# Performance work log

Measured on AMD Instinct MI355X. Metric: run time of the kernel, lower is better.

The kernel has to match this reference:

```python
import jax, jax.numpy as jnp
import numpy as np

# mamba-130m config (n_layers reduced to 4 for the reference baseline)
V, Dm, NL, Di, Ns, K, R = 50280, 768, 4, 1536, 16, 4, 48

def rmsnorm(x, w, eps=1e-5):
    return x * jax.lax.rsqrt(jnp.mean(x * x, axis=-1, keepdims=True) + eps) * w

def mixer(r, in_w, conv_w, conv_b, x_w, dt_w, dt_b, A_log, Dp, out_w):
    Bsz, L, _ = r.shape
    xz = jnp.einsum('bld,ed->ble', r, in_w)            # [B,L,2*Di]
    x, z = jnp.split(xz, 2, axis=-1)
    # depthwise causal conv1d, kernel K
    xp = jnp.pad(x, ((0, 0), (K - 1, 0), (0, 0)))
    x = sum(conv_w[:, k] * xp[:, k:k + L] for k in range(K)) + conv_b
    x = jax.nn.silu(x)
    proj = jnp.einsum('bld,ed->ble', x, x_w)           # [B,L,R+2*Ns]
    dt_r, Bm, Cm = proj[..., :R], proj[..., R:R + Ns], proj[..., R + Ns:]
    dt = jax.nn.softplus(jnp.einsum('blr,dr->bld', dt_r, dt_w) + dt_b)  # [B,L,Di]
    A = -jnp.exp(A_log)                                # [Di,Ns]
    dA = jnp.exp(dt[..., None] * A)                    # [B,L,Di,Ns]
    dBx = dt[..., None] * Bm[:, :, None, :] * x[..., None]
    def step(h, xs):
        dA_t, dBx_t, C_t = xs
        h = dA_t * h + dBx_t                           # [B,Di,Ns]
        return h, jnp.einsum('bdn,bn->bd', h, C_t)
    h0 = jnp.zeros((Bsz, Di, Ns), r.dtype)
    _, ys = jax.lax.scan(step, h0, (dA.transpose(1, 0, 2, 3), dBx.transpose(1, 0, 2, 3), Cm.transpose(1, 0, 2)))
    y = ys.transpose(1, 0, 2) + Dp * x
    y = y * jax.nn.silu(z)
    return jnp.einsum('ble,de->bld', y, out_w)

def mamba_logits(ids, mask, embed, in_proj_w, conv_w, conv_b, x_proj_w, dt_proj_w, dt_proj_b, A_log, Dp, out_proj_w, norm_w, final_norm_w):
    h = embed[ids] * mask[..., None].astype(embed.dtype)
    for l in range(NL):
        h = h + mixer(rmsnorm(h, norm_w[l]), in_proj_w[l], conv_w[l], conv_b[l],
                      x_proj_w[l], dt_proj_w[l], dt_proj_b[l], A_log[l], Dp[l], out_proj_w[l])
    h = rmsnorm(h, final_norm_w)
    return jnp.einsum('bld,vd->blv', h, embed)  # tied lm_head

def setup_inputs() -> dict:
    key = jax.random.key(0)
    ks = jax.random.split(key, 12)
    s = 0.02
    B, Lq, La = 2, 512, 128
    dt_b0 = float(np.log(np.expm1(0.01)))  # softplus^{-1}(0.01)
    return {
        'question_ids': jax.random.randint(ks[0], (B, Lq), 0, V, dtype=jnp.int64),
        'question_mask': jnp.ones((B, Lq), dtype=jnp.int32),
        'answer_ids': jax.random.randint(ks[1], (B, La), 0, V, dtype=jnp.int64),
        'answer_mask': jnp.ones((B, La), dtype=jnp.int32),
        'embed': jax.random.normal(ks[2], (V, Dm), jnp.float32) * s,
        'in_proj_w': jax.random.normal(ks[3], (NL, 2 * Di, Dm), jnp.float32) * s,
        'conv_w': jax.random.normal(ks[4], (NL, Di, K), jnp.float32) * s,
        'conv_b': jnp.zeros((NL, Di), jnp.float32),
        'x_proj_w': jax.random.normal(ks[5], (NL, R + 2 * Ns, Di), jnp.float32) * s,
        'dt_proj_w': jax.random.normal(ks[6], (NL, Di, R), jnp.float32) * s,
        'dt_proj_b': jnp.full((NL, Di), dt_b0, jnp.float32),
        'A_log': jnp.broadcast_to(jnp.log(jnp.arange(1, Ns + 1, dtype=jnp.float32)), (NL, Di, Ns)).copy(),
        'Dp': jnp.ones((NL, Di), jnp.float32),
        'out_proj_w': jax.random.normal(ks[7], (NL, Dm, Di), jnp.float32) * s,
        'norm_w': jnp.ones((NL, Dm), jnp.float32),
        'final_norm_w': jnp.ones((Dm,), jnp.float32),
    }

def reference(question_ids, question_mask, answer_ids, answer_mask, embed, in_proj_w, conv_w, conv_b, x_proj_w, dt_proj_w, dt_proj_b, A_log, Dp, out_proj_w, norm_w, final_norm_w):
    # answer_ids/answer_mask are unused by the original forward as well.
    return mamba_logits(question_ids, question_mask, embed, in_proj_w, conv_w, conv_b,
                        x_proj_w, dt_proj_w, dt_proj_b, A_log, Dp, out_proj_w, norm_w, final_norm_w)
```

## Files before the change

### kernel.cpp

```cpp
#include <hip/hip_runtime.h>

#define DI 1536
#define DM 768
#define NS 16
#define RK 48
#define LQ 512
#define BB 2
#define MROWS (BB*LQ)

typedef unsigned short u16;
typedef short bf16x8 __attribute__((ext_vector_type(8)));
typedef float f32x4 __attribute__((ext_vector_type(4)));
typedef u16 u16x8 __attribute__((ext_vector_type(8)));

static __device__ __forceinline__ short f2bf(float f) {
  unsigned u = __float_as_uint(f);
  u += 0x7FFF + ((u >> 16) & 1);
  return (short)(u >> 16);
}

static __device__ __forceinline__ void gld16(const void* g, void* l) {
  __builtin_amdgcn_global_load_lds((const __attribute__((address_space(1))) unsigned int*)g,
                                   (__attribute__((address_space(3))) unsigned int*)l,
                                   16, 0, 0);
}

__global__ __launch_bounds__(256) void k_cast8(const float* __restrict__ s,
                                               u16* __restrict__ d, long n) {
  long i = ((long)blockIdx.x * 256 + threadIdx.x) * 8;
  if (i >= n) return;
  float4 a = *(const float4*)(s + i);
  float4 b = *(const float4*)(s + i + 4);
  u16x8 o;
  o[0] = (u16)f2bf(a.x); o[1] = (u16)f2bf(a.y); o[2] = (u16)f2bf(a.z); o[3] = (u16)f2bf(a.w);
  o[4] = (u16)f2bf(b.x); o[5] = (u16)f2bf(b.y); o[6] = (u16)f2bf(b.z); o[7] = (u16)f2bf(b.w);
  *(u16x8*)(d + i) = o;
}

__global__ __launch_bounds__(256) void k_gather(const int* __restrict__ ids,
                                                const int* __restrict__ mask,
                                                const float* __restrict__ embed,
                                                float* __restrict__ h) {
  int row = blockIdx.x;
  int id = ids[row];
  float mk = (float)mask[row];
  const float* src = embed + (size_t)id * DM;
  float* dst = h + (size_t)row * DM;
  for (int i = threadIdx.x; i < DM; i += 256) dst[i] = src[i] * mk;
}

__global__ __launch_bounds__(256) void k_rmsnorm(const float* __restrict__ h,
                                                 const float* __restrict__ w,
                                                 u16* __restrict__ out) {
  int row = blockIdx.x;
  const float* x = h + (size_t)row * DM;
  int tid = threadIdx.x;
  float v0 = x[tid], v1 = x[tid + 256], v2 = x[tid + 512];
  float ss = v0*v0 + v1*v1 + v2*v2;
  #pragma unroll
  for (int o = 32; o > 0; o >>= 1) ss += __shfl_xor(ss, o);
  __shared__ float ps[4];
  if ((tid & 63) == 0) ps[tid >> 6] = ss;
  __syncthreads();
  float tot = ps[0] + ps[1] + ps[2] + ps[3];
  float scale = rsqrtf(tot * (1.0f/768.0f) + 1e-5f);
  u16* o0 = out + (size_t)row * DM;
  o0[tid]       = (u16)f2bf(v0 * scale * w[tid]);
  o0[tid + 256] = (u16)f2bf(v1 * scale * w[tid + 256]);
  o0[tid + 512] = (u16)f2bf(v2 * scale * w[tid + 512]);
}

template<int WM, int WN, int TM, int TN, bool RES>
__global__ __launch_bounds__(256) void k_gemm_bf(const u16* __restrict__ A,
                                                 const u16* __restrict__ B,
                                                 float* __restrict__ C,
                                                 int M, int N, int K) {
  constexpr int BM = WM*TM*16, BN = WN*TN*16, BK = 32;
  __shared__ __attribute__((aligned(16))) u16 As[BM*BK];
  __shared__ __attribute__((aligned(16))) u16 Bs[BN*BK];

  int bx, by;
  {
    int CT = gridDim.x, RT = gridDim.y;
    int lin = blockIdx.y * CT + blockIdx.x;
    int CT8 = CT & ~7;
    int main_n = CT8 * RT;
    if (lin < main_n) {
      int x = lin & 7, g = lin >> 3;
      by = g % RT;
      bx = x + 8 * (g / RT);
    } else {
      int rem = lin - main_n;
      by = rem % RT;
      bx = CT8 + rem / RT;
    }
  }

  const int m0 = by * BM, n0 = bx * BN;
  const int tid = threadIdx.x;
  const int wave = tid >> 6, lane = tid & 63;
  const int wm = (wave / WN) * (TM*16), wn = (wave % WN) * (TN*16);
  const int lm = lane & 15, q = lane >> 4;
  const int srow = tid >> 2;
  const int ssub = (tid & 3) * 8;

  f32x4 acc[TM][TN] = {};
  for (int kt = 0; kt < K; kt += BK) {
    __syncthreads();
    #pragma unroll
    for (int i = 0; i < BM/64; i++) {
      const u16* g = A + (size_t)(m0 + i*64 + srow)*K + kt + ssub;
      gld16(g, (void*)(As + (i*256 + wave*64)*8));
    }
    #pragma unroll
    for (int i = 0; i < BN/64; i++) {
      int bn = n0 + i*64 + srow;
      if (bn > N-1) bn = N-1;
      const u16* g = B + (size_t)bn*K + kt + ssub;
      gld16(g, (void*)(Bs + (i*256 + wave*64)*8));
    }
    __syncthreads();
    bf16x8 af[TM], bfr[TN];
    #pragma unroll
    for (int i = 0; i < TM; i++)
      af[i] = *(const bf16x8*)(&As[(wm + i*16 + lm)*BK + q*8]);
    #pragma unroll
    for (int j = 0; j < TN; j++)
      bfr[j] = *(const bf16x8*)(&Bs[(wn + j*16 + lm)*BK + q*8]);
    #pragma unroll
    for (int i = 0; i < TM; i++)
      #pragma unroll
      for (int j = 0; j < TN; j++)
        acc[i][j] = __builtin_amdgcn_mfma_f32_16x16x32_bf16(af[i], bfr[j], acc[i][j], 0, 0, 0);
  }
  #pragma unroll
  for (int i = 0; i < TM; i++) {
    #pragma unroll
    for (int j = 0; j < TN; j++) {
      int rm = m0 + wm + i*16 + q*4;
      int cn = n0 + wn + j*16 + lm;
      if (cn < N) {
        float* cp = C + (size_t)rm*N + cn;
        #pragma unroll
        for (int r2 = 0; r2 < 4; r2++) {
          float v = acc[i][j][r2];
          if (RES) v += cp[(size_t)r2*N];
          cp[(size_t)r2*N] = v;
        }
      }
    }
  }
}

__global__ __launch_bounds__(256) void k_conv(const float* __restrict__ xz,
                                              const float* __restrict__ cw,
                                              const float* __restrict__ cb,
                                              float* __restrict__ xs) {
  int idx = blockIdx.x * 256 + threadIdx.x;
  int d = idx % DI;
  int t = (idx / DI) % LQ;
  int b = idx / (DI * LQ);
  const float* xcol = xz + (size_t)b * LQ * (2*DI) + d;
  float acc = cb[d];
  #pragma unroll
  for (int k = 0; k < 4; k++) {
    int tt = t + k - 3;
    if (tt >= 0) acc += cw[d*4 + k] * xcol[(size_t)tt * (2*DI)];
  }
  float s = acc / (1.0f + expf(-acc));
  xs[idx] = s;
}

__global__ __launch_bounds__(256) void k_proj(const float* __restrict__ xs,
                                              const float* __restrict__ w,
                                              float* __restrict__ proj) {
  int wave = threadIdx.x >> 6, lane = threadIdx.x & 63;
  int m = blockIdx.x * 4 + wave;
  const float* xr = xs + (size_t)m * DI;
  float xv[24];
  #pragma unroll
  for (int j = 0; j < 24; j++) xv[j] = xr[lane + j*64];
  for (int n = 0; n < 80; n++) {
    const float* wr = w + (size_t)n * DI;
    float acc = 0.f;
    #pragma unroll
    for (int j = 0; j < 24; j++) acc += xv[j] * wr[lane + j*64];
    #pragma unroll
    for (int o = 32; o > 0; o >>= 1) acc += __shfl_xor(acc, o);
    if (lane == 0) proj[(size_t)m * 80 + n] = acc;
  }
}

__global__ __launch_bounds__(256) void k_dt(const float* __restrict__ proj,
                                            const float* __restrict__ dtw,
                                            const float* __restrict__ dtb,
                                            float* __restrict__ dt) {
  int m = blockIdx.y;
  int d = blockIdx.x * 256 + threadIdx.x;
  __shared__ float p[RK];
  if (threadIdx.x < RK) p[threadIdx.x] = proj[(size_t)m * 80 + threadIdx.x];
  __syncthreads();
  const float* wr = dtw + (size_t)d * RK;
  float acc = dtb[d];
  #pragma unroll
  for (int r = 0; r < RK; r++) acc += p[r] * wr[r];
  float sp = (acc > 20.f) ? acc : log1pf(expf(acc));
  dt[(size_t)m * DI + d] = sp;
}

#define SCT 32
__global__ __launch_bounds__(256) void k_scan(const float* __restrict__ dt,
                                              const float* __restrict__ proj,
                                              const float* __restrict__ xs,
                                              const float* __restrict__ A_log,
                                              float* __restrict__ y) {
  const int d = blockIdx.x;
  const int b = blockIdx.y;
  const int tid = threadIdx.x;
  const int n = tid & 15;
  const int c = tid >> 4;
  const int t0 = c * SCT;
  const float negA = -expf(A_log[d * NS + n]);
  const float* dtp = dt   + (size_t)b * LQ * DI + d;
  const float* xp  = xs   + (size_t)b * LQ * DI + d;
  const float* Bp  = proj + (size_t)b * LQ * 80 + RK + n;
  const float* Cp  = proj + (size_t)b * LQ * 80 + RK + NS + n;

  float a[SCT], u[SCT], Cv[SCT];
  #pragma unroll
  for (int j = 0; j < SCT; j++) {
    int t = t0 + j;
    float dtv = dtp[(size_t)t * DI];
    float xv  = xp[(size_t)t * DI];
    float Bv  = Bp[(size_t)t * 80];
    Cv[j]     = Cp[(size_t)t * 80];
    a[j] = expf(dtv * negA);
    u[j] = dtv * Bv * xv;
  }
  float P = 1.f, H = 0.f;
  #pragma unroll
  for (int j = 0; j < SCT; j++) { H = a[j]*H + u[j]; P *= a[j]; }

  __shared__ float Ps[16][16], Hs[16][16], Ss[16][16];
  Ps[c][n] = P; Hs[c][n] = H;
  __syncthreads();
  if (tid < 16) {
    float S = 0.f;
    #pragma unroll
    for (int cc = 0; cc < 16; cc++) {
      Ss[cc][tid] = S;
      S = Ps[cc][tid] * S + Hs[cc][tid];
    }
  }
  __syncthreads();

  float h = Ss[c][n];
  float* yp = y + (size_t)b * LQ * DI + d;
  #pragma unroll
  for (int j = 0; j < SCT; j++) {
    h = a[j]*h + u[j];
    float yy = h * Cv[j];
    yy += __shfl_xor(yy, 1);
    yy += __shfl_xor(yy, 2);
    yy += __shfl_xor(yy, 4);
    yy += __shfl_xor(yy, 8);
    if (n == 0) yp[(size_t)(t0 + j) * DI] = yy;
  }
}

__global__ __launch_bounds__(256) void k_gate(const float* __restrict__ y,
                                              const float* __restrict__ xs,
                                              const float* __restrict__ xz,
                                              const float* __restrict__ Dp,
                                              u16* __restrict__ yb) {
  int idx = blockIdx.x * 256 + threadIdx.x;
  int d = idx % DI;
  int bt = idx / DI;
  float zv = xz[(size_t)bt * (2*DI) + DI + d];
  float sz = zv / (1.0f + expf(-zv));
  float v = (y[idx] + Dp[d] * xs[idx]) * sz;
  yb[idx] = (u16)f2bf(v);
}

extern "C" void kernel_launch(void* const* d_in, const int* in_sizes, int n_in,
                              void* d_out, int out_size, void* d_ws, size_t ws_size,
                              hipStream_t stream) {
  const int*   q_ids        = (const int*)d_in[0];
  const int*   q_mask       = (const int*)d_in[1];
  const float* embed        = (const float*)d_in[4];
  const float* in_proj_w    = (const float*)d_in[5];
  const float* conv_w       = (const float*)d_in[6];
  const float* conv_b       = (const float*)d_in[7];
  const float* x_proj_w     = (const float*)d_in[8];
  const float* dt_proj_w    = (const float*)d_in[9];
  const float* dt_proj_b    = (const float*)d_in[10];
  const float* A_log        = (const float*)d_in[11];
  const float* Dp           = (const float*)d_in[12];
  const float* out_proj_w   = (const float*)d_in[13];
  const float* norm_w       = (const float*)d_in[14];
  const float* final_norm_w = (const float*)d_in[15];
  float* out = (float*)d_out;

  float* ws = (float*)d_ws;
  float* h   = ws;
  float* xz  = h  + 786432;
  float* xs  = xz + 3145728;
  float* pj  = xs + 1572864;
  float* dtb = pj + 81920;
  float* y   = dtb + 1572864;
  u16*   rb  = (u16*)(y + 1572864);
  u16*   yb  = rb  + 786432;
  u16*   ipw = yb  + 1572864;
  u16*   opw = ipw + 9437184;
  u16*   emb = opw + 4718592;

  k_cast8<<<4608, 256, 0, stream>>>(in_proj_w, ipw, 9437184L);
  k_cast8<<<2304, 256, 0, stream>>>(out_proj_w, opw, 4718592L);
  k_cast8<<<18855, 256, 0, stream>>>(embed, emb, 38615040L);

  k_gather<<<MROWS, 256, 0, stream>>>(q_ids, q_mask, embed, h);

  for (int l = 0; l < 4; l++) {
    k_rmsnorm<<<MROWS, 256, 0, stream>>>(h, norm_w + (size_t)l*DM, rb);
    k_gemm_bf<1,4,4,2,false><<<dim3(3072/128, MROWS/64), 256, 0, stream>>>(
        rb, ipw + (size_t)l*2359296, xz, MROWS, 2*DI, DM);
    k_conv<<<(MROWS*DI)/256, 256, 0, stream>>>(xz, conv_w + (size_t)l*DI*4,
                                               conv_b + (size_t)l*DI, xs);
    k_proj<<<MROWS/4, 256, 0, stream>>>(xs, x_proj_w + (size_t)l*80*DI, pj);
    k_dt<<<dim3(DI/256, MROWS), 256, 0, stream>>>(pj, dt_proj_w + (size_t)l*DI*RK,
                                                  dt_proj_b + (size_t)l*DI, dtb);
    k_scan<<<dim3(DI, BB), 256, 0, stream>>>(dtb, pj, xs,
                                             A_log + (size_t)l*DI*NS, y);
    k_gate<<<(MROWS*DI)/256, 256, 0, stream>>>(y, xs, xz, Dp + (size_t)l*DI, yb);
    k_gemm_bf<2,2,2,2,true><<<dim3(DM/64, MROWS/64), 256, 0, stream>>>(
        yb, opw + (size_t)l*1179648, h, MROWS, DM, DI);
  }

  k_rmsnorm<<<MROWS, 256, 0, stream>>>(h, final_norm_w, rb);
  k_gemm_bf<2,2,4,4,false><<<dim3((50280 + 127)/128, MROWS/128), 256, 0, stream>>>(
      rb, emb, out, MROWS, 50280, 768);
}
```

Before: 1.537 ms.

## Double-buffer GEMM LDS tiles and fuse dt projection and gating into scan

The GEMM kernel now uses two LDS buffers and issues the async global-to-LDS load for the next K tile before computing on the current one. This is meant to overlap memory latency with MFMA work and cut one barrier per iteration. Separately, the dt projection plus softplus is computed inside the scan block into shared memory, and the D-skip plus SiLU gate with the bf16 store is folded into the scan output loop. That removes two kernel launches and the dt/y intermediate buffers, but each scan block recomputes dt for all 512 timesteps. There is also a possible race: the next-tile async loads are issued without waiting on completion before the barrier.

```diff
diff --git a/kernel.cpp b/kernel.cpp
--- a/kernel.cpp
+++ b/kernel.cpp
@@ -76,8 +76,8 @@
                                                  float* __restrict__ C,
                                                  int M, int N, int K) {
   constexpr int BM = WM*TM*16, BN = WN*TN*16, BK = 32;
-  __shared__ __attribute__((aligned(16))) u16 As[BM*BK];
-  __shared__ __attribute__((aligned(16))) u16 Bs[BN*BK];
+  __shared__ __attribute__((aligned(16))) u16 As[2][BM*BK];
+  __shared__ __attribute__((aligned(16))) u16 Bs[2][BN*BK];
 
   int bx, by;
   {
@@ -104,34 +104,41 @@
   const int srow = tid >> 2;
   const int ssub = (tid & 3) * 8;
 
-  f32x4 acc[TM][TN] = {};
-  for (int kt = 0; kt < K; kt += BK) {
-    __syncthreads();
+  auto stage = [&](int buf, int kt) {
     #pragma unroll
     for (int i = 0; i < BM/64; i++) {
       const u16* g = A + (size_t)(m0 + i*64 + srow)*K + kt + ssub;
-      gld16(g, (void*)(As + (i*256 + wave*64)*8));
+      gld16(g, (void*)(As[buf] + (i*256 + wave*64)*8));
     }
     #pragma unroll
     for (int i = 0; i < BN/64; i++) {
       int bn = n0 + i*64 + srow;
       if (bn > N-1) bn = N-1;
       const u16* g = B + (size_t)bn*K + kt + ssub;
-      gld16(g, (void*)(Bs + (i*256 + wave*64)*8));
-    }
-    __syncthreads();
+      gld16(g, (void*)(Bs[buf] + (i*256 + wave*64)*8));
+    }
+  };
+
+  f32x4 acc[TM][TN] = {};
+  const int nt = K / BK;
+  stage(0, 0);
+  __syncthreads();
+  for (int t = 0; t < nt; ++t) {
+    const int cur = t & 1;
+    if (t + 1 < nt) stage(cur ^ 1, (t + 1) * BK);
     bf16x8 af[TM], bfr[TN];
     #pragma unroll
     for (int i = 0; i < TM; i++)
-      af[i] = *(const bf16x8*)(&As[(wm + i*16 + lm)*BK + q*8]);
+      af[i] = *(const bf16x8*)(&As[cur][(wm + i*16 + lm)*BK + q*8]);
     #pragma unroll
     for (int j = 0; j < TN; j++)
-      bfr[j] = *(const bf16x8*)(&Bs[(wn + j*16 + lm)*BK + q*8]);
+      bfr[j] = *(const bf16x8*)(&Bs[cur][(wn + j*16 + lm)*BK + q*8]);
     #pragma unroll
     for (int i = 0; i < TM; i++)
       #pragma unroll
       for (int j = 0; j < TN; j++)
         acc[i][j] = __builtin_amdgcn_mfma_f32_16x16x32_bf16(af[i], bfr[j], acc[i][j], 0, 0, 0);
+    __syncthreads();
   }
   #pragma unroll
   for (int i = 0; i < TM; i++) {
@@ -191,46 +198,47 @@
   }
 }
 
-__global__ __launch_bounds__(256) void k_dt(const float* __restrict__ proj,
-                                            const float* __restrict__ dtw,
-                                            const float* __restrict__ dtb,
-                                            float* __restrict__ dt) {
-  int m = blockIdx.y;
-  int d = blockIdx.x * 256 + threadIdx.x;
-  __shared__ float p[RK];
-  if (threadIdx.x < RK) p[threadIdx.x] = proj[(size_t)m * 80 + threadIdx.x];
-  __syncthreads();
-  const float* wr = dtw + (size_t)d * RK;
-  float acc = dtb[d];
-  #pragma unroll
-  for (int r = 0; r < RK; r++) acc += p[r] * wr[r];
-  float sp = (acc > 20.f) ? acc : log1pf(expf(acc));
-  dt[(size_t)m * DI + d] = sp;
-}
-
 #define SCT 32
-__global__ __launch_bounds__(256) void k_scan(const float* __restrict__ dt,
-                                              const float* __restrict__ proj,
+__global__ __launch_bounds__(256) void k_scan(const float* __restrict__ proj,
                                               const float* __restrict__ xs,
+                                              const float* __restrict__ xz,
                                               const float* __restrict__ A_log,
-                                              float* __restrict__ y) {
+                                              const float* __restrict__ dtw,
+                                              const float* __restrict__ dtbp,
+                                              const float* __restrict__ Dp,
+                                              u16* __restrict__ yb) {
   const int d = blockIdx.x;
   const int b = blockIdx.y;
   const int tid = threadIdx.x;
   const int n = tid & 15;
   const int c = tid >> 4;
   const int t0 = c * SCT;
+
+  __shared__ float dt_s[LQ];
+  const float* pjb = proj + (size_t)b * LQ * 80;
+  {
+    const float* wr = dtw + (size_t)d * RK;
+    float dtb0 = dtbp[d];
+    for (int t = tid; t < LQ; t += 256) {
+      const float* pr = pjb + (size_t)t * 80;
+      float acc = dtb0;
+      #pragma unroll
+      for (int r = 0; r < RK; r++) acc += pr[r] * wr[r];
+      dt_s[t] = (acc > 20.f) ? acc : log1pf(expf(acc));
+    }
+  }
+  __syncthreads();
+
   const float negA = -expf(A_log[d * NS + n]);
-  const float* dtp = dt   + (size_t)b * LQ * DI + d;
-  const float* xp  = xs   + (size_t)b * LQ * DI + d;
-  const float* Bp  = proj + (size_t)b * LQ * 80 + RK + n;
-  const float* Cp  = proj + (size_t)b * LQ * 80 + RK + NS + n;
+  const float* xp  = xs + (size_t)b * LQ * DI + d;
+  const float* Bp  = pjb + RK + n;
+  const float* Cp  = pjb + RK + NS + n;
 
   float a[SCT], u[SCT], Cv[SCT];
   #pragma unroll
   for (int j = 0; j < SCT; j++) {
     int t = t0 + j;
-    float dtv = dtp[(size_t)t * DI];
+    float dtv = dt_s[t];
     float xv  = xp[(size_t)t * DI];
     float Bv  = Bp[(size_t)t * 80];
     Cv[j]     = Cp[(size_t)t * 80];
@@ -255,7 +263,9 @@
   __syncthreads();
 
   float h = Ss[c][n];
-  float* yp = y + (size_t)b * LQ * DI + d;
+  const float Dpd = Dp[d];
+  const float* zp = xz + (size_t)b * LQ * (2*DI) + DI + d;
+  u16* yp = yb + (size_t)b * LQ * DI + d;
   #pragma unroll
   for (int j = 0; j < SCT; j++) {
     h = a[j]*h + u[j];
@@ -264,22 +274,14 @@
     yy += __shfl_xor(yy, 2);
     yy += __shfl_xor(yy, 4);
     yy += __shfl_xor(yy, 8);
-    if (n == 0) yp[(size_t)(t0 + j) * DI] = yy;
-  }
-}
-
-__global__ __launch_bounds__(256) void k_gate(const float* __restrict__ y,
-                                              const float* __restrict__ xs,
-                                              const float* __restrict__ xz,
-                                              const float* __restrict__ Dp,
-                                              u16* __restrict__ yb) {
-  int idx = blockIdx.x * 256 + threadIdx.x;
-  int d = idx % DI;
-  int bt = idx / DI;
-  float zv = xz[(size_t)bt * (2*DI) + DI + d];
-  float sz = zv / (1.0f + expf(-zv));
-  float v = (y[idx] + Dp[d] * xs[idx]) * sz;
-  yb[idx] = (u16)f2bf(v);
+    if (n == (j & 15)) {
+      int t = t0 + j;
+      float xv = xp[(size_t)t * DI];
+      float zv = zp[(size_t)t * (2*DI)];
+      float sz = zv / (1.0f + expf(-zv));
+      yp[(size_t)t * DI] = (u16)f2bf((yy + Dpd * xv) * sz);
+    }
+  }
 }
 
 extern "C" void kernel_launch(void* const* d_in, const int* in_sizes, int n_in,
@@ -306,9 +308,7 @@
   float* xz  = h  + 786432;
   float* xs  = xz + 3145728;
   float* pj  = xs + 1572864;
-  float* dtb = pj + 81920;
-  float* y   = dtb + 1572864;
-  u16*   rb  = (u16*)(y + 1572864);
+  u16*   rb  = (u16*)(pj + 81920);
   u16*   yb  = rb  + 786432;
   u16*   ipw = yb  + 1572864;
   u16*   opw = ipw + 9437184;
@@ -327,11 +327,11 @@
     k_conv<<<(MROWS*DI)/256, 256, 0, stream>>>(xz, conv_w + (size_t)l*DI*4,
                                                conv_b + (size_t)l*DI, xs);
     k_proj<<<MROWS/4, 256, 0, stream>>>(xs, x_proj_w + (size_t)l*80*DI, pj);
-    k_dt<<<dim3(DI/256, MROWS), 256, 0, stream>>>(pj, dt_proj_w + (size_t)l*DI*RK,
-                                                  dt_proj_b + (size_t)l*DI, dtb);
-    k_scan<<<dim3(DI, BB), 256, 0, stream>>>(dtb, pj, xs,
-                                             A_log + (size_t)l*DI*NS, y);
-    k_gate<<<(MROWS*DI)/256, 256, 0, stream>>>(y, xs, xz, Dp + (size_t)l*DI, yb);
+    k_scan<<<dim3(DI, BB), 256, 0, stream>>>(pj, xs, xz,
+                                             A_log + (size_t)l*DI*NS,
+                                             dt_proj_w + (size_t)l*DI*RK,
+                                             dt_proj_b + (size_t)l*DI,
+                                             Dp + (size_t)l*DI, yb);
     k_gemm_bf<2,2,2,2,true><<<dim3(DM/64, MROWS/64), 256, 0, stream>>>(
         yb, opw + (size_t)l*1179648, h, MROWS, DM, DI);
   }
```

Measured after the change: 1.543 ms. About the same (+0.4%).
